# Kernel optimization log

Hardware: AMD Instinct MI355X
Metric: run time of the kernel (lower is better)

The kernel has to match this reference:

```python
import jax, jax.numpy as jnp
import numpy as np

B, L, D, H = 4, 2048, 512, 8
DK = D // H


def setup_inputs() -> dict:
    key = jax.random.key(0)
    ks = jax.random.split(key, 12)
    s = 1.0 / np.sqrt(D)
    return {
        "q": jax.random.normal(ks[0], (B, L, D), jnp.float32),
        "k": jax.random.normal(ks[1], (B, L, D), jnp.float32),
        "v": jax.random.normal(ks[2], (B, L, D), jnp.float32),
        "masks": jax.random.randint(ks[3], (B, L), 0, 2, jnp.int32),
        "wq_w": jax.random.normal(ks[4], (D, D), jnp.float32) * s,
        "wq_b": jnp.zeros((D,), jnp.float32),
        "wk_w": jax.random.normal(ks[5], (D, D), jnp.float32) * s,
        "wk_b": jnp.zeros((D,), jnp.float32),
        "wv_w": jax.random.normal(ks[6], (D, D), jnp.float32) * s,
        "wv_b": jnp.zeros((D,), jnp.float32),
        "wo_w": jax.random.normal(ks[7], (D, D), jnp.float32) * s,
        "wo_b": jnp.zeros((D,), jnp.float32),
    }


def reference(q, k, v, masks, wq_w, wq_b, wk_w, wk_b, wv_w, wv_b, wo_w, wo_b):
    b, l1, d = q.shape
    l2 = k.shape[1]
    # torch Linear: y = x @ W.T + b; weight shape (out, in)
    qh = (q @ wq_w.T + wq_b).reshape(b, l1, H, DK).transpose(0, 2, 1, 3)  # (B,H,L1,DK)
    kh = (k @ wk_w.T + wk_b).reshape(b, l2, H, DK).transpose(0, 2, 1, 3)  # (B,H,L2,DK)
    vh = (v @ wv_w.T + wv_b).reshape(b, l2, H, DK).transpose(0, 2, 1, 3)  # (B,H,L2,DK)
    scores = jnp.einsum("bhqd,bhkd->bhqk", qh, kh) / np.sqrt(DK).astype(np.float32)
    # 2D encoder mask (B, L2) broadcast over heads and query positions
    neg = jnp.float32(np.finfo(np.float32).min)
    scores = jnp.where(masks[:, None, None, :] == 0, neg, scores)
    weights = jax.nn.softmax(scores, axis=-1)  # dropout_rate=0.0 -> identity
    ctx = jnp.einsum("bhqk,bhkd->bhqd", weights, vh)
    concat = ctx.transpose(0, 2, 1, 3).reshape(b, l1, d)
    return concat @ wo_w.T + wo_b
```

## Files before the change

### kernel.cpp

```cpp
#include <hip/hip_runtime.h>
#include <hip/hip_bf16.h>
#include <cstddef>

typedef __attribute__((ext_vector_type(8)))  short bf16x8;
typedef __attribute__((ext_vector_type(4)))  float f32x4;

constexpr int Bn = 4, Ln = 2048, Dn = 512, Hn = 8, DKn = 64, Mtot = 8192;
constexpr float QSCALE = 0.125f * 1.44269504088896341f;
constexpr size_t HE = (size_t)Bn * Hn * Ln * DKn;
constexpr size_t WN = (size_t)Dn * Dn;

__device__ inline unsigned cvt_pk_bf16(float lo, float hi) {
    unsigned r;
    asm("v_cvt_pk_bf16_f32 %0, %1, %2" : "=v"(r) : "v"(lo), "v"(hi));
    return r;
}
__device__ inline short f2bf(float x) {
    union { float f; unsigned u; } v; v.f = x;
    unsigned r = v.u + 0x7fffu + ((v.u >> 16) & 1u);
    return (short)(r >> 16);
}
__device__ inline void gl_lds16(const short* g, short* l) {
    __builtin_amdgcn_global_load_lds(
        (const __attribute__((address_space(1))) void*)g,
        (__attribute__((address_space(3))) void*)l, 16, 0, 0);
}

__global__ __launch_bounds__(256) void prep_all(
    const float* __restrict__ q, const float* __restrict__ k, const float* __restrict__ v,
    const float* __restrict__ wq, const float* __restrict__ wk,
    const float* __restrict__ wv, const float* __restrict__ wo,
    const int* __restrict__ masks,
    short* __restrict__ Xb, short* __restrict__ Wb, float* __restrict__ maskF)
{
    const size_t NX4 = 3 * HE / 4;
    const size_t NW4 = WN;
    size_t gid = (size_t)blockIdx.x * 256 + threadIdx.x;
    if (gid < NX4) {
        const size_t per = HE / 4;
        int which = (int)(gid >> 20);
        const float* src = (which == 0) ? q : (which == 1) ? k : v;
        size_t i4 = gid & (per - 1);
        float4 xv = *(const float4*)&src[i4 * 4];
        uint2 p = {cvt_pk_bf16(xv.x, xv.y), cvt_pk_bf16(xv.z, xv.w)};
        *(uint2*)&Xb[(size_t)which * HE + i4 * 4] = p;
    } else if (gid < NX4 + NW4) {
        size_t wi4 = gid - NX4;
        const size_t per = WN / 4;
        int which = (int)(wi4 >> 16);
        const float* src = (which == 0) ? wq : (which == 1) ? wk : (which == 2) ? wv : wo;
        size_t i4 = wi4 & (per - 1);
        float4 xv = *(const float4*)&src[i4 * 4];
        uint2 p = {cvt_pk_bf16(xv.x, xv.y), cvt_pk_bf16(xv.z, xv.w)};
        *(uint2*)&Wb[(size_t)which * WN + i4 * 4] = p;
    } else {
        size_t mi = gid - NX4 - NW4;
        if (mi < (size_t)Bn * Ln) maskF[mi] = (masks[mi] == 0) ? -1e30f : 0.f;
    }
}

__global__ __launch_bounds__(256) void mask_prep(
    const int* __restrict__ masks, float* __restrict__ maskF)
{
    int i = blockIdx.x * 256 + threadIdx.x;
    if (i < Bn * Ln) maskF[i] = (masks[i] == 0) ? -1e30f : 0.f;
}

__global__ __launch_bounds__(256) void qkv_proj_bf16(
    const short* __restrict__ Xb, const short* __restrict__ Wb,
    const float* __restrict__ bq, const float* __restrict__ bk, const float* __restrict__ bv,
    short* __restrict__ Qh, short* __restrict__ Kh, short* __restrict__ Vt)
{
    const int p = blockIdx.z;
    const short* X    = Xb + (size_t)p * Mtot * Dn;
    const short* W    = Wb + (size_t)p * Dn * Dn;
    const float* bias = (p == 0) ? bq : (p == 1) ? bk : bv;
    short*       O    = (p == 0) ? Qh : (p == 1) ? Kh : Vt;
    const float scl   = (p == 0) ? QSCALE : 1.0f;

    __shared__ short As[128 * 64];
    __shared__ short Bs[128 * 64];

    const int tid  = threadIdx.x;
    const int lane = tid & 63, w = tid >> 6;
    const int wr = w >> 1, wc = w & 1;
    const int l16 = lane & 15, g = lane >> 4;
    const int m0 = blockIdx.x * 128, n0 = blockIdx.y * 128;

    const short* Ag[4]; const short* Bg[4]; int ldsOff[4];
    #pragma unroll
    for (int f = 0; f < 4; ++f) {
        int c = tid + 256 * f;
        int row = c >> 3, col8 = c & 7;
        int scolw = ((col8 ^ (row & 7)) << 3);
        Ag[f] = X + (size_t)(m0 + row) * Dn + scolw;
        Bg[f] = W + (size_t)(n0 + row) * Dn + scolw;
        ldsOff[f] = (w * 64 + 256 * f) * 8;
    }

    f32x4 acc[4][4];
    #pragma unroll
    for (int i = 0; i < 4; ++i)
        #pragma unroll
        for (int j = 0; j < 4; ++j)
            acc[i][j] = (f32x4){0.f, 0.f, 0.f, 0.f};

    for (int ks = 0; ks < 8; ++ks) {
        #pragma unroll
        for (int f = 0; f < 4; ++f) {
            gl_lds16(Ag[f], &As[ldsOff[f]]);
            gl_lds16(Bg[f], &Bs[ldsOff[f]]);
            Ag[f] += 64; Bg[f] += 64;
        }
        __syncthreads();

        bf16x8 bfv[4][2];
        #pragma unroll
        for (int j = 0; j < 4; ++j) {
            int row = wc * 64 + j * 16 + l16;
            int sw = (row & 7) << 3;
            bfv[j][0] = *(const bf16x8*)&Bs[row * 64 + ((g * 8) ^ sw)];
            bfv[j][1] = *(const bf16x8*)&Bs[row * 64 + ((32 + g * 8) ^ sw)];
        }
        #pragma unroll
        for (int i = 0; i < 4; ++i) {
            int row = wr * 64 + i * 16 + l16;
            int sw = (row & 7) << 3;
            bf16x8 a0 = *(const bf16x8*)&As[row * 64 + ((g * 8) ^ sw)];
            bf16x8 a1 = *(const bf16x8*)&As[row * 64 + ((32 + g * 8) ^ sw)];
            #pragma unroll
            for (int j = 0; j < 4; ++j) {
                acc[i][j] = __builtin_amdgcn_mfma_f32_16x16x32_bf16(a0, bfv[j][0], acc[i][j], 0, 0, 0);
                acc[i][j] = __builtin_amdgcn_mfma_f32_16x16x32_bf16(a1, bfv[j][1], acc[i][j], 0, 0, 0);
            }
        }
        __syncthreads();
    }

    const int bb = m0 >> 11;
    #pragma unroll
    for (int i = 0; i < 4; ++i) {
        #pragma unroll
        for (int j = 0; j < 4; ++j) {
            int n  = n0 + wc * 64 + j * 16 + l16;
            int h  = n >> 6, dk = n & 63;
            float bval = bias[n];
            #pragma unroll
            for (int r = 0; r < 4; ++r) {
                int m  = m0 + wr * 64 + i * 16 + g * 4 + r;
                int lq = m & (Ln - 1);
                short val = f2bf((acc[i][j][r] + bval) * scl);
                if (p < 2)
                    O[(((size_t)bb * Hn + h) * Ln + lq) * DKn + dk] = val;
                else
                    O[(((size_t)bb * Hn + h) * DKn + dk) * Ln + lq] = val;
            }
        }
    }
}

__global__ __launch_bounds__(256) void out_proj_bf16(
    const short* __restrict__ Ctx, const short* __restrict__ Wo,
    const float* __restrict__ bias, float* __restrict__ Out)
{
    __shared__ short As[64 * 64];
    __shared__ short Bs[64 * 64];

    const int tid  = threadIdx.x;
    const int lane = tid & 63, w = tid >> 6;
    const int wr = w >> 1, wc = w & 1;
    const int l16 = lane & 15, g = lane >> 4;
    const int m0 = blockIdx.x * 64, n0 = blockIdx.y * 64;

    const short* Ag[2]; const short* Bg[2]; int ldsOff[2];
    #pragma unroll
    for (int f = 0; f < 2; ++f) {
        int c = tid + 256 * f;
        int row = c >> 3, col8 = c & 7;
        int scolw = ((col8 ^ (row & 7)) << 3);
        Ag[f] = Ctx + (size_t)(m0 + row) * Dn + scolw;
        Bg[f] = Wo  + (size_t)(n0 + row) * Dn + scolw;
        ldsOff[f] = (w * 64 + 256 * f) * 8;
    }

    f32x4 acc[2][2];
    #pragma unroll
    for (int i = 0; i < 2; ++i)
        #pragma unroll
        for (int j = 0; j < 2; ++j)
            acc[i][j] = (f32x4){0.f, 0.f, 0.f, 0.f};

    for (int ks = 0; ks < 8; ++ks) {
        #pragma unroll
        for (int f = 0; f < 2; ++f) {
            gl_lds16(Ag[f], &As[ldsOff[f]]);
            gl_lds16(Bg[f], &Bs[ldsOff[f]]);
            Ag[f] += 64; Bg[f] += 64;
        }
        __syncthreads();

        bf16x8 bfv[2][2];
        #pragma unroll
        for (int j = 0; j < 2; ++j) {
            int row = wc * 32 + j * 16 + l16;
            int sw = (row & 7) << 3;
            bfv[j][0] = *(const bf16x8*)&Bs[row * 64 + ((g * 8) ^ sw)];
            bfv[j][1] = *(const bf16x8*)&Bs[row * 64 + ((32 + g * 8) ^ sw)];
        }
        #pragma unroll
        for (int i = 0; i < 2; ++i) {
            int row = wr * 32 + i * 16 + l16;
            int sw = (row & 7) << 3;
            bf16x8 a0 = *(const bf16x8*)&As[row * 64 + ((g * 8) ^ sw)];
            bf16x8 a1 = *(const bf16x8*)&As[row * 64 + ((32 + g * 8) ^ sw)];
            #pragma unroll
            for (int j = 0; j < 2; ++j) {
                acc[i][j] = __builtin_amdgcn_mfma_f32_16x16x32_bf16(a0, bfv[j][0], acc[i][j], 0, 0, 0);
                acc[i][j] = __builtin_amdgcn_mfma_f32_16x16x32_bf16(a1, bfv[j][1], acc[i][j], 0, 0, 0);
            }
        }
        __syncthreads();
    }

    #pragma unroll
    for (int i = 0; i < 2; ++i) {
        #pragma unroll
        for (int j = 0; j < 2; ++j) {
            int n = n0 + wc * 32 + j * 16 + l16;
            float bval = bias[n];
            #pragma unroll
            for (int r = 0; r < 4; ++r) {
                int m = m0 + wr * 32 + i * 16 + g * 4 + r;
                Out[(size_t)m * Dn + n] = acc[i][j][r] + bval;
            }
        }
    }
}

__global__ __launch_bounds__(256, 3) void attn_mfma(
    const short* __restrict__ Qh, const short* __restrict__ Kh, const short* __restrict__ Vt,
    const float* __restrict__ maskF, short* __restrict__ Ctx)
{
    __shared__ short smem[16384];

    const int tid  = threadIdx.x;
    const int lane = tid & 63, w = tid >> 6;
    const int l16 = lane & 15, g = lane >> 4;
    const int qt = w & 1, hf = w >> 1;

    const int bid = blockIdx.x;
    const int id  = (bid & 7) * 128 + (bid >> 3);
    const int qb  = id & 31;
    const int bh  = id >> 5;
    const int bb  = bh >> 3, hd = bh & 7;
    const int q0  = qb * 64;
    constexpr int NT = 32;

    const short* Qp = Qh + (size_t)bh * Ln * DKn;
    const short* Kp = Kh + (size_t)bh * Ln * DKn;
    const short* Vp = Vt + (size_t)bh * DKn * Ln;
    const float* mp = maskF + bb * Ln + hf * 1024;

    bf16x8 qf[2][2];
    #pragma unroll
    for (int mf = 0; mf < 2; ++mf)
        #pragma unroll
        for (int c = 0; c < 2; ++c)
            qf[mf][c] = *(const bf16x8*)&Qp[(size_t)(q0 + qt * 32 + mf * 16 + l16) * DKn + c * 32 + g * 8];

    constexpr short BF1 = (short)0x3F80;
    const bf16x8 ones = {BF1, BF1, BF1, BF1, BF1, BF1, BF1, BF1};

    const short* kg[2]; const short* vg[2]; int sbk[2];
    #pragma unroll
    for (int j = 0; j < 2; ++j) {
        int sb = qt * 2 + j;
        sbk[j] = sb * 512;
        int p  = sb * 8 + (lane >> 3);
        int kc = ((p & 0x0C) << 1) | ((p & 0x10) >> 2) | (p & 3);
        int scol = ((lane & 7) ^ (p & 7)) << 3;
        kg[j] = Kp + (size_t)(hf * 1024 + kc) * DKn + scol;
        int vrow = sb * 16 + (lane >> 2);
        int scolv = (((lane & 3) ^ (vrow & 3)) << 3);
        vg[j] = Vp + (size_t)vrow * Ln + hf * 1024 + scolv;
    }

    int kofs[2][2];
    #pragma unroll
    for (int kt = 0; kt < 2; ++kt) {
        int row = kt * 16 + l16;
        kofs[kt][0] = row * 64 + ((g * 8) ^ ((row & 7) << 3));
        kofs[kt][1] = row * 64 + ((32 + g * 8) ^ ((row & 7) << 3));
    }
    int vofs[4];
    #pragma unroll
    for (int d = 0; d < 4; ++d)
        vofs[d] = (d * 16 + l16) * 32 + ((g * 8) ^ ((l16 & 3) << 3));

    f32x4 oacc[2][4];
    #pragma unroll
    for (int mf = 0; mf < 2; ++mf)
        #pragma unroll
        for (int d = 0; d < 4; ++d) oacc[mf][d] = (f32x4){0.f, 0.f, 0.f, 0.f};
    f32x4 lsum[2] = {(f32x4){0.f, 0.f, 0.f, 0.f}, (f32x4){0.f, 0.f, 0.f, 0.f}};

    #pragma unroll
    for (int j = 0; j < 2; ++j) {
        gl_lds16(kg[j], smem + hf * 4096 + sbk[j]);
        gl_lds16(vg[j], smem + 8192 + hf * 4096 + sbk[j]);
    }
    __syncthreads();

    int cb = 0;
    for (int t = 0; t < NT; ++t) {
        if (t < NT - 1) {
            const int ko = (t + 1) * 2048;
            const int vo = (t + 1) * 32;
            short* kd = smem + (hf * 2 + (cb ^ 1)) * 2048;
            short* vd = smem + 8192 + (hf * 2 + (cb ^ 1)) * 2048;
            #pragma unroll
            for (int j = 0; j < 2; ++j) {
                gl_lds16(kg[j] + ko, kd + sbk[j]);
                gl_lds16(vg[j] + vo, vd + sbk[j]);
            }
        }
        const short* Kb = smem + (hf * 2 + cb) * 2048;
        const short* Vb = smem + 8192 + (hf * 2 + cb) * 2048;

        f32x4 mk[2];
        mk[0] = *(const f32x4*)&mp[t * 32 + 8 * g];
        mk[1] = *(const f32x4*)&mp[t * 32 + 8 * g + 4];

        bf16x8 kf[2][2];
        #pragma unroll
        for (int kt = 0; kt < 2; ++kt) {
            kf[kt][0] = *(const bf16x8*)&Kb[kofs[kt][0]];
            kf[kt][1] = *(const bf16x8*)&Kb[kofs[kt][1]];
        }

        f32x4 sv[2][2];
        __builtin_amdgcn_s_setprio(1);
        #pragma unroll
        for (int mf = 0; mf < 2; ++mf)
            #pragma unroll
            for (int kt = 0; kt < 2; ++kt) {
                f32x4 z = __builtin_amdgcn_mfma_f32_16x16x32_bf16(kf[kt][0], qf[mf][0], mk[kt], 0, 0, 0);
                z = __builtin_amdgcn_mfma_f32_16x16x32_bf16(kf[kt][1], qf[mf][1], z, 0, 0, 0);
                sv[mf][kt] = z;
            }
        __builtin_amdgcn_s_setprio(0);

        bf16x8 pf[2];
        #pragma unroll
        for (int mf = 0; mf < 2; ++mf) {
            float e0 = exp2f(sv[mf][0][0]), e1 = exp2f(sv[mf][0][1]);
            float e2 = exp2f(sv[mf][0][2]), e3 = exp2f(sv[mf][0][3]);
            float e4 = exp2f(sv[mf][1][0]), e5 = exp2f(sv[mf][1][1]);
            float e6 = exp2f(sv[mf][1][2]), e7 = exp2f(sv[mf][1][3]);
            union { unsigned u[4]; bf16x8 v; } pu;
            pu.u[0] = cvt_pk_bf16(e0, e1);
            pu.u[1] = cvt_pk_bf16(e2, e3);
            pu.u[2] = cvt_pk_bf16(e4, e5);
            pu.u[3] = cvt_pk_bf16(e6, e7);
            pf[mf] = pu.v;
        }

        bf16x8 vf[4];
        #pragma unroll
        for (int d = 0; d < 4; ++d)
            vf[d] = *(const bf16x8*)&Vb[vofs[d]];

        __builtin_amdgcn_s_setprio(1);
        #pragma unroll
        for (int mf = 0; mf < 2; ++mf) {
            lsum[mf] = __builtin_amdgcn_mfma_f32_16x16x32_bf16(ones, pf[mf], lsum[mf], 0, 0, 0);
            #pragma unroll
            for (int d = 0; d < 4; ++d)
                oacc[mf][d] = __builtin_amdgcn_mfma_f32_16x16x32_bf16(vf[d], pf[mf], oacc[mf][d], 0, 0, 0);
        }
        __builtin_amdgcn_s_setprio(0);

        __syncthreads();
        cb ^= 1;
    }

    float* M = (float*)smem;
    if (hf == 1) {
        #pragma unroll
        for (int mf = 0; mf < 2; ++mf) {
            int ql = qt * 32 + mf * 16 + l16;
            #pragma unroll
            for (int d = 0; d < 4; ++d)
                *(f32x4*)&M[ql * 68 + d * 16 + g * 4] = oacc[mf][d];
            if (g == 0) M[ql * 68 + 64] = lsum[mf][0];
        }
    }
    __syncthreads();
    if (hf == 0) {
        #pragma unroll
        for (int mf = 0; mf < 2; ++mf) {
            int ql = qt * 32 + mf * 16 + l16;
            float lt = lsum[mf][0] + M[ql * 68 + 64];
            float inv = 1.0f / lt;
            size_t mrow = (size_t)bb * Ln + q0 + ql;
            #pragma unroll
            for (int d = 0; d < 4; ++d) {
                f32x4 ob = *(const f32x4*)&M[ql * 68 + d * 16 + g * 4];
                float o0 = (oacc[mf][d][0] + ob[0]) * inv;
                float o1 = (oacc[mf][d][1] + ob[1]) * inv;
                float o2 = (oacc[mf][d][2] + ob[2]) * inv;
                float o3 = (oacc[mf][d][3] + ob[3]) * inv;
                uint2 pr = {cvt_pk_bf16(o0, o1), cvt_pk_bf16(o2, o3)};
                *(uint2*)&Ctx[mrow * Dn + hd * 64 + d * 16 + g * 4] = pr;
            }
        }
    }
}

__global__ __launch_bounds__(256) void qkv_proj_mfma(
    const float* __restrict__ q, const float* __restrict__ k, const float* __restrict__ v,
    const float* __restrict__ wq, const float* __restrict__ wk, const float* __restrict__ wv,
    const float* __restrict__ bq, const float* __restrict__ bk, const float* __restrict__ bv,
    short* __restrict__ Qh, short* __restrict__ Kh, short* __restrict__ Vt)
{
    const int p = blockIdx.z;
    const float* X    = (p == 0) ? q  : (p == 1) ? k  : v;
    const float* W    = (p == 0) ? wq : (p == 1) ? wk : wv;
    const float* bias = (p == 0) ? bq : (p == 1) ? bk : bv;
    short*       O    = (p == 0) ? Qh : (p == 1) ? Kh : Vt;
    const float scl   = (p == 0) ? QSCALE : 1.0f;

    __shared__ short As[128 * 72];
    __shared__ short Bs[128 * 72];

    const int tid  = threadIdx.x;
    const int lane = tid & 63, w = tid >> 6;
    const int wr = w >> 1, wc = w & 1;
    const int l16 = lane & 15, g = lane >> 4;
    const int m0 = blockIdx.x * 128, n0 = blockIdx.y * 128;

    f32x4 acc[4][4];
    #pragma unroll
    for (int i = 0; i < 4; ++i)
        #pragma unroll
        for (int j = 0; j < 4; ++j)
            acc[i][j] = (f32x4){0.f, 0.f, 0.f, 0.f};

    for (int k0 = 0; k0 < Dn; k0 += 64) {
        #pragma unroll
        for (int f = 0; f < 8; ++f) {
            int lin = tid + 256 * f;
            int row = lin >> 4, c4 = lin & 15;
            float4 xv = *(const float4*)&X[(size_t)(m0 + row) * Dn + k0 + c4 * 4];
            uint2 xp = {cvt_pk_bf16(xv.x, xv.y), cvt_pk_bf16(xv.z, xv.w)};
            *(uint2*)&As[row * 72 + c4 * 4] = xp;
            float4 wv4 = *(const float4*)&W[(size_t)(n0 + row) * Dn + k0 + c4 * 4];
            uint2 wp = {cvt_pk_bf16(wv4.x, wv4.y), cvt_pk_bf16(wv4.z, wv4.w)};
            *(uint2*)&Bs[row * 72 + c4 * 4] = wp;
        }
        __syncthreads();

        bf16x8 af[4][2], bfv[4][2];
        #pragma unroll
        for (int i = 0; i < 4; ++i)
            #pragma unroll
            for (int c = 0; c < 2; ++c)
                af[i][c] = *(const bf16x8*)&As[(wr * 64 + i * 16 + l16) * 72 + c * 32 + g * 8];
        #pragma unroll
        for (int j = 0; j < 4; ++j)
            #pragma unroll
            for (int c = 0; c < 2; ++c)
                bfv[j][c] = *(const bf16x8*)&Bs[(wc * 64 + j * 16 + l16) * 72 + c * 32 + g * 8];

        #pragma unroll
        for (int i = 0; i < 4; ++i)
            #pragma unroll
            for (int j = 0; j < 4; ++j) {
                acc[i][j] = __builtin_amdgcn_mfma_f32_16x16x32_bf16(af[i][0], bfv[j][0], acc[i][j], 0, 0, 0);
                acc[i][j] = __builtin_amdgcn_mfma_f32_16x16x32_bf16(af[i][1], bfv[j][1], acc[i][j], 0, 0, 0);
            }
        __syncthreads();
    }

    const int bb = m0 >> 11;
    #pragma unroll
    for (int i = 0; i < 4; ++i) {
        #pragma unroll
        for (int j = 0; j < 4; ++j) {
            int n  = n0 + wc * 64 + j * 16 + l16;
            int h  = n >> 6, dk = n & 63;
            float bval = bias[n];
            #pragma unroll
            for (int r = 0; r < 4; ++r) {
                int m  = m0 + wr * 64 + i * 16 + g * 4 + r;
                int lq = m & (Ln - 1);
                short val = f2bf((acc[i][j][r] + bval) * scl);
                if (p < 2)
                    O[(((size_t)bb * Hn + h) * Ln + lq) * DKn + dk] = val;
                else
                    O[(((size_t)bb * Hn + h) * DKn + dk) * Ln + lq] = val;
            }
        }
    }
}

__global__ __launch_bounds__(256) void out_proj_mfma(
    const short* __restrict__ Ctx, const float* __restrict__ W,
    const float* __restrict__ bias, float* __restrict__ Out)
{
    __shared__ short As[128 * 72];
    __shared__ short Bs[128 * 72];

    const int tid  = threadIdx.x;
    const int lane = tid & 63, w = tid >> 6;
    const int wr = w >> 1, wc = w & 1;
    const int l16 = lane & 15, g = lane >> 4;
    const int m0 = blockIdx.x * 128, n0 = blockIdx.y * 128;

    f32x4 acc[4][4];
    #pragma unroll
    for (int i = 0; i < 4; ++i)
        #pragma unroll
        for (int j = 0; j < 4; ++j)
            acc[i][j] = (f32x4){0.f, 0.f, 0.f, 0.f};

    for (int k0 = 0; k0 < Dn; k0 += 64) {
        #pragma unroll
        for (int f = 0; f < 4; ++f) {
            int lin = tid + 256 * f;
            int row = lin >> 3, c8 = lin & 7;
            bf16x8 av = *(const bf16x8*)&Ctx[(size_t)(m0 + row) * Dn + k0 + c8 * 8];
            *(bf16x8*)&As[row * 72 + c8 * 8] = av;
        }
        #pragma unroll
        for (int f = 0; f < 8; ++f) {
            int lin = tid + 256 * f;
            int row = lin >> 4, c4 = lin & 15;
            float4 wv4 = *(const float4*)&W[(size_t)(n0 + row) * Dn + k0 + c4 * 4];
            uint2 wp = {cvt_pk_bf16(wv4.x, wv4.y), cvt_pk_bf16(wv4.z, wv4.w)};
            *(uint2*)&Bs[row * 72 + c4 * 4] = wp;
        }
        __syncthreads();

        bf16x8 af[4][2], bfv[4][2];
        #pragma unroll
        for (int i = 0; i < 4; ++i)
            #pragma unroll
            for (int c = 0; c < 2; ++c)
                af[i][c] = *(const bf16x8*)&As[(wr * 64 + i * 16 + l16) * 72 + c * 32 + g * 8];
        #pragma unroll
        for (int j = 0; j < 4; ++j)
            #pragma unroll
            for (int c = 0; c < 2; ++c)
                bfv[j][c] = *(const bf16x8*)&Bs[(wc * 64 + j * 16 + l16) * 72 + c * 32 + g * 8];

        #pragma unroll
        for (int i = 0; i < 4; ++i)
            #pragma unroll
            for (int j = 0; j < 4; ++j) {
                acc[i][j] = __builtin_amdgcn_mfma_f32_16x16x32_bf16(af[i][0], bfv[j][0], acc[i][j], 0, 0, 0);
                acc[i][j] = __builtin_amdgcn_mfma_f32_16x16x32_bf16(af[i][1], bfv[j][1], acc[i][j], 0, 0, 0);
            }
        __syncthreads();
    }

    #pragma unroll
    for (int i = 0; i < 4; ++i) {
        #pragma unroll
        for (int j = 0; j < 4; ++j) {
            int n = n0 + wc * 64 + j * 16 + l16;
            float bval = bias[n];
            #pragma unroll
            for (int r = 0; r < 4; ++r) {
                int m = m0 + wr * 64 + i * 16 + g * 4 + r;
                Out[(size_t)m * Dn + n] = acc[i][j][r] + bval;
            }
        }
    }
}

extern "C" void kernel_launch(void* const* d_in, const int* in_sizes, int n_in,
                              void* d_out, int out_size, void* d_ws, size_t ws_size,
                              hipStream_t stream)
{
    (void)in_sizes; (void)n_in; (void)out_size;
    const float* q    = (const float*)d_in[0];
    const float* k    = (const float*)d_in[1];
    const float* v    = (const float*)d_in[2];
    const int*   mks  = (const int*)  d_in[3];
    const float* wq_w = (const float*)d_in[4];
    const float* wq_b = (const float*)d_in[5];
    const float* wk_w = (const float*)d_in[6];
    const float* wk_b = (const float*)d_in[7];
    const float* wv_w = (const float*)d_in[8];
    const float* wv_b = (const float*)d_in[9];
    const float* wo_w = (const float*)d_in[10];
    const float* wo_b = (const float*)d_in[11];
    float* out = (float*)d_out;

    short* ws = (short*)d_ws;
    const size_t needed = (6 * HE + 4 * WN + 2 * (size_t)Bn * Ln) * 2;

    if (ws_size >= needed) {
        short* Xb   = ws;
        short* Ctx  = ws;
        short* Qh   = ws + 3 * HE;
        short* Kh   = ws + 4 * HE;
        short* Vt   = ws + 5 * HE;
        short* Wb   = ws + 6 * HE;
        float* maskF = (float*)(ws + 6 * HE + 4 * WN);

        const int prepBlocks = (int)((3 * HE / 4 + WN + (size_t)Bn * Ln + 255) / 256);
        prep_all<<<dim3(prepBlocks), 256, 0, stream>>>(
            q, k, v, wq_w, wk_w, wv_w, wo_w, mks, Xb, Wb, maskF);

        qkv_proj_bf16<<<dim3(64, 4, 3), 256, 0, stream>>>(
            Xb, Wb, wq_b, wk_b, wv_b, Qh, Kh, Vt);

        attn_mfma<<<dim3(1024), 256, 0, stream>>>(Qh, Kh, Vt, maskF, Ctx);

        out_proj_bf16<<<dim3(128, 8), 256, 0, stream>>>(Ctx, Wb + 3 * WN, wo_b, out);
    } else {
        short* Qh  = ws;
        short* Kh  = ws + HE;
        short* Vt  = ws + 2 * HE;
        short* Ctx = ws + 3 * HE;
        float* maskF = (float*)(ws + 4 * HE);

        mask_prep<<<dim3(32), 256, 0, stream>>>(mks, maskF);
        qkv_proj_mfma<<<dim3(Mtot / 128, Dn / 128, 3), 256, 0, stream>>>(
            q, k, v, wq_w, wk_w, wv_w, wq_b, wk_b, wv_b, Qh, Kh, Vt);
        attn_mfma<<<dim3(1024), 256, 0, stream>>>(Qh, Kh, Vt, maskF, Ctx);
        out_proj_mfma<<<dim3(Mtot / 128, Dn / 128), 256, 0, stream>>>(Ctx, wo_w, wo_b, out);
    }
}
```

Baseline: 114.0 us.

## Fuse fp32-to-bf16 activation conversion into QKV projection GEMM

Removes the separate pass that converted q/k/v to bf16 in workspace. The QKV GEMM now loads fp32 activation tiles straight into LDS and converts them to bf16 in registers before the MFMA. This removes a full read/write round trip of the activations and shrinks the workspace. In exchange, each GEMM block loads twice the A-tile bytes, uses more LDS (which may reduce occupancy), and does the conversion repeatedly across column blocks.

```diff
diff --git a/kernel.cpp b/kernel.cpp
--- a/kernel.cpp
+++ b/kernel.cpp
@@ -25,36 +25,28 @@
         (const __attribute__((address_space(1))) void*)g,
         (__attribute__((address_space(3))) void*)l, 16, 0, 0);
 }
-
-__global__ __launch_bounds__(256) void prep_all(
-    const float* __restrict__ q, const float* __restrict__ k, const float* __restrict__ v,
+__device__ inline void gl_lds16f(const float* g, float* l) {
+    __builtin_amdgcn_global_load_lds(
+        (const __attribute__((address_space(1))) void*)g,
+        (__attribute__((address_space(3))) void*)l, 16, 0, 0);
+}
+
+__global__ __launch_bounds__(256) void prep_wm(
     const float* __restrict__ wq, const float* __restrict__ wk,
     const float* __restrict__ wv, const float* __restrict__ wo,
     const int* __restrict__ masks,
-    short* __restrict__ Xb, short* __restrict__ Wb, float* __restrict__ maskF)
-{
-    const size_t NX4 = 3 * HE / 4;
-    const size_t NW4 = WN;
+    short* __restrict__ Wb, float* __restrict__ maskF)
+{
     size_t gid = (size_t)blockIdx.x * 256 + threadIdx.x;
-    if (gid < NX4) {
-        const size_t per = HE / 4;
-        int which = (int)(gid >> 20);
-        const float* src = (which == 0) ? q : (which == 1) ? k : v;
-        size_t i4 = gid & (per - 1);
-        float4 xv = *(const float4*)&src[i4 * 4];
-        uint2 p = {cvt_pk_bf16(xv.x, xv.y), cvt_pk_bf16(xv.z, xv.w)};
-        *(uint2*)&Xb[(size_t)which * HE + i4 * 4] = p;
-    } else if (gid < NX4 + NW4) {
-        size_t wi4 = gid - NX4;
-        const size_t per = WN / 4;
-        int which = (int)(wi4 >> 16);
+    if (gid < WN) {
+        int which = (int)(gid >> 16);
         const float* src = (which == 0) ? wq : (which == 1) ? wk : (which == 2) ? wv : wo;
-        size_t i4 = wi4 & (per - 1);
+        size_t i4 = gid & 65535;
         float4 xv = *(const float4*)&src[i4 * 4];
         uint2 p = {cvt_pk_bf16(xv.x, xv.y), cvt_pk_bf16(xv.z, xv.w)};
         *(uint2*)&Wb[(size_t)which * WN + i4 * 4] = p;
     } else {
-        size_t mi = gid - NX4 - NW4;
+        size_t mi = gid - WN;
         if (mi < (size_t)Bn * Ln) maskF[mi] = (masks[mi] == 0) ? -1e30f : 0.f;
     }
 }
@@ -66,19 +58,20 @@
     if (i < Bn * Ln) maskF[i] = (masks[i] == 0) ? -1e30f : 0.f;
 }
 
-__global__ __launch_bounds__(256) void qkv_proj_bf16(
-    const short* __restrict__ Xb, const short* __restrict__ Wb,
+__global__ __launch_bounds__(256) void qkv_proj_f32(
+    const float* __restrict__ q, const float* __restrict__ k, const float* __restrict__ v,
+    const short* __restrict__ Wb,
     const float* __restrict__ bq, const float* __restrict__ bk, const float* __restrict__ bv,
     short* __restrict__ Qh, short* __restrict__ Kh, short* __restrict__ Vt)
 {
     const int p = blockIdx.z;
-    const short* X    = Xb + (size_t)p * Mtot * Dn;
-    const short* W    = Wb + (size_t)p * Dn * Dn;
+    const float* X    = (p == 0) ? q : (p == 1) ? k : v;
+    const short* W    = Wb + (size_t)p * WN;
     const float* bias = (p == 0) ? bq : (p == 1) ? bk : bv;
     short*       O    = (p == 0) ? Qh : (p == 1) ? Kh : Vt;
     const float scl   = (p == 0) ? QSCALE : 1.0f;
 
-    __shared__ short As[128 * 64];
+    __shared__ float Af[128 * 64];
     __shared__ short Bs[128 * 64];
 
     const int tid  = threadIdx.x;
@@ -87,16 +80,12 @@
     const int l16 = lane & 15, g = lane >> 4;
     const int m0 = blockIdx.x * 128, n0 = blockIdx.y * 128;
 
-    const short* Ag[4]; const short* Bg[4]; int ldsOff[4];
-    #pragma unroll
-    for (int f = 0; f < 4; ++f) {
-        int c = tid + 256 * f;
-        int row = c >> 3, col8 = c & 7;
-        int scolw = ((col8 ^ (row & 7)) << 3);
-        Ag[f] = X + (size_t)(m0 + row) * Dn + scolw;
-        Bg[f] = W + (size_t)(n0 + row) * Dn + scolw;
-        ldsOff[f] = (w * 64 + 256 * f) * 8;
-    }
+    const int rA = tid >> 4, col4 = tid & 15;
+    const int scolA = (col4 * 4) ^ (8 * (rA & 7));
+    const float* Ag = X + (size_t)(m0 + rA) * Dn + scolA;
+    const int rB = tid >> 3, c8 = tid & 7;
+    const int scolB = ((c8 ^ (rB & 7)) << 3);
+    const short* Bg = W + (size_t)(n0 + rB) * Dn + scolB;
 
     f32x4 acc[4][4];
     #pragma unroll
@@ -107,11 +96,12 @@
 
     for (int ks = 0; ks < 8; ++ks) {
         #pragma unroll
-        for (int f = 0; f < 4; ++f) {
-            gl_lds16(Ag[f], &As[ldsOff[f]]);
-            gl_lds16(Bg[f], &Bs[ldsOff[f]]);
-            Ag[f] += 64; Bg[f] += 64;
-        }
+        for (int f = 0; f < 8; ++f)
+            gl_lds16f(Ag + (size_t)f * 16 * Dn, &Af[(w * 64 + 256 * f) * 4]);
+        #pragma unroll
+        for (int f = 0; f < 4; ++f)
+            gl_lds16(Bg + (size_t)f * 32 * Dn, &Bs[(w * 64 + 256 * f) * 8]);
+        Ag += 64; Bg += 64;
         __syncthreads();
 
         bf16x8 bfv[4][2];
@@ -125,13 +115,24 @@
         #pragma unroll
         for (int i = 0; i < 4; ++i) {
             int row = wr * 64 + i * 16 + l16;
-            int sw = (row & 7) << 3;
-            bf16x8 a0 = *(const bf16x8*)&As[row * 64 + ((g * 8) ^ sw)];
-            bf16x8 a1 = *(const bf16x8*)&As[row * 64 + ((32 + g * 8) ^ sw)];
+            int m8 = 8 * (row & 7);
+            bf16x8 a[2];
+            #pragma unroll
+            for (int c = 0; c < 2; ++c) {
+                int base = row * 64 + ((g * 8 + c * 32) ^ m8);
+                f32x4 x0 = *(const f32x4*)&Af[base];
+                f32x4 x1 = *(const f32x4*)&Af[base + 4];
+                union { unsigned u[4]; bf16x8 v; } pu;
+                pu.u[0] = cvt_pk_bf16(x0[0], x0[1]);
+                pu.u[1] = cvt_pk_bf16(x0[2], x0[3]);
+                pu.u[2] = cvt_pk_bf16(x1[0], x1[1]);
+                pu.u[3] = cvt_pk_bf16(x1[2], x1[3]);
+                a[c] = pu.v;
+            }
             #pragma unroll
             for (int j = 0; j < 4; ++j) {
-                acc[i][j] = __builtin_amdgcn_mfma_f32_16x16x32_bf16(a0, bfv[j][0], acc[i][j], 0, 0, 0);
-                acc[i][j] = __builtin_amdgcn_mfma_f32_16x16x32_bf16(a1, bfv[j][1], acc[i][j], 0, 0, 0);
+                acc[i][j] = __builtin_amdgcn_mfma_f32_16x16x32_bf16(a[0], bfv[j][0], acc[i][j], 0, 0, 0);
+                acc[i][j] = __builtin_amdgcn_mfma_f32_16x16x32_bf16(a[1], bfv[j][1], acc[i][j], 0, 0, 0);
             }
         }
         __syncthreads();
@@ -599,23 +600,22 @@
     float* out = (float*)d_out;
 
     short* ws = (short*)d_ws;
-    const size_t needed = (6 * HE + 4 * WN + 2 * (size_t)Bn * Ln) * 2;
+    const size_t needed = (4 * HE + 4 * WN + 2 * (size_t)Bn * Ln) * 2;
 
     if (ws_size >= needed) {
-        short* Xb   = ws;
-        short* Ctx  = ws;
-        short* Qh   = ws + 3 * HE;
-        short* Kh   = ws + 4 * HE;
-        short* Vt   = ws + 5 * HE;
-        short* Wb   = ws + 6 * HE;
-        float* maskF = (float*)(ws + 6 * HE + 4 * WN);
-
-        const int prepBlocks = (int)((3 * HE / 4 + WN + (size_t)Bn * Ln + 255) / 256);
-        prep_all<<<dim3(prepBlocks), 256, 0, stream>>>(
-            q, k, v, wq_w, wk_w, wv_w, wo_w, mks, Xb, Wb, maskF);
-
-        qkv_proj_bf16<<<dim3(64, 4, 3), 256, 0, stream>>>(
-            Xb, Wb, wq_b, wk_b, wv_b, Qh, Kh, Vt);
+        short* Qh   = ws;
+        short* Kh   = ws + HE;
+        short* Vt   = ws + 2 * HE;
+        short* Ctx  = ws + 3 * HE;
+        short* Wb   = ws + 4 * HE;
+        float* maskF = (float*)(ws + 4 * HE + 4 * WN);
+
+        const int prepBlocks = (int)((WN + (size_t)Bn * Ln + 255) / 256);
+        prep_wm<<<dim3(prepBlocks), 256, 0, stream>>>(
+            wq_w, wk_w, wv_w, wo_w, mks, Wb, maskF);
+
+        qkv_proj_f32<<<dim3(64, 4, 3), 256, 0, stream>>>(
+            q, k, v, Wb, wq_b, wk_b, wv_b, Qh, Kh, Vt);
 
         attn_mfma<<<dim3(1024), 256, 0, stream>>>(Qh, Kh, Vt, maskF, Ctx);
 
```

Measured after the change: 114.0 us. No clear change (+0.0%).
